# Performance work log

Measured on AMD Instinct MI355X. Metric: run time of the kernel, lower is better.

## Reference

```python
import jax, jax.numpy as jnp
import numpy as np

M = 8192          # flattened tokens (batch*seq)
IN_FEATURES = 4096
OUT_FEATURES = 4096


def setup_inputs() -> dict:
    key = jax.random.key(0)
    k1, k2, k3 = jax.random.split(key, 3)
    # int8-valued activations and weights, stored as int32 (values in [-128, 127])
    x = jax.random.randint(k1, (M, IN_FEATURES), -128, 128, dtype=jnp.int32)
    int_weight = jax.random.randint(k2, (OUT_FEATURES, IN_FEATURES), -128, 127, dtype=jnp.int32)
    bias = (jax.random.normal(k3, (OUT_FEATURES,), dtype=jnp.float32) * 0.02).astype(jnp.float16)
    return {"x": x, "int_weight": int_weight, "bias": bias}


def reference(x, int_weight, bias):
    # x.to(torch.int8); quik int8Matmul: int8 GEMM with int32 accumulation, out = x @ W^T
    x_i8 = x.astype(jnp.int8)
    w_i8 = int_weight.astype(jnp.int8)
    acc = jax.lax.dot_general(
        x_i8, w_i8,
        dimension_numbers=(((1,), (1,)), ((), ())),  # [M, K] x [N, K] -> [M, N]
        preferred_element_type=jnp.int32,
    )
    # .to(torch.float16) then bias add (fused epilogue target)
    return acc.astype(jnp.float16) + bias
```

## Files before the change

kernel.cpp:

```cpp
#include <hip/hip_runtime.h>

#define MDIM 8192
#define NDIM 4096
#define KDIM 4096
#define BM 256
#define BN 128
#define BK 128

typedef int v4i __attribute__((ext_vector_type(4)));
typedef int v16i __attribute__((ext_vector_type(16)));

__device__ __forceinline__ unsigned pack4(int x, int y, int z, int w) {
    return (unsigned)(x & 0xff) | ((unsigned)(y & 0xff) << 8) |
           ((unsigned)(z & 0xff) << 16) | ((unsigned)w << 24);
}

__global__ __launch_bounds__(256) void pack_tiled(const int* __restrict__ x,
                                                  const int* __restrict__ w,
                                                  uint4* __restrict__ xp,
                                                  uint4* __restrict__ wp) {
    __shared__ unsigned lds32[256 * 33];
    const int wg  = blockIdx.x;
    const int tid = threadIdx.x;
    const int kq   = tid & 31;
    const int rsub = tid >> 5;

    if (wg < 1024) {
        const int mtile = wg >> 5, kiter = wg & 31;
        const int* base = x + (size_t)(mtile * 256) * KDIM + kiter * 128;
#pragma unroll
        for (int it = 0; it < 32; ++it) {
            const int row = it * 8 + rsub;
            int4 v = *(const int4*)(base + (size_t)row * KDIM + kq * 4);
            lds32[row * 33 + kq] = pack4(v.x, v.y, v.z, v.w);
        }
        __syncthreads();
        uint4* dst = xp + (size_t)(mtile * 32 + kiter) * 2048;
#pragma unroll
        for (int it = 0; it < 8; ++it) {
            const int g = it * 256 + tid;
            const int kb = g >> 8, row = g & 255;
            const unsigned* p = &lds32[row * 33 + kb * 4];
            uint4 o;
            o.x = p[0]; o.y = p[1]; o.z = p[2]; o.w = p[3];
            dst[g] = o;
        }
    } else {
        const int ntile = (wg - 1024) >> 5, kiter = wg & 31;
        const int* base = w + (size_t)(ntile * 128) * KDIM + kiter * 128;
#pragma unroll
        for (int it = 0; it < 16; ++it) {
            const int row = it * 8 + rsub;
            int4 v = *(const int4*)(base + (size_t)row * KDIM + kq * 4);
            lds32[row * 33 + kq] = pack4(v.x, v.y, v.z, v.w);
        }
        __syncthreads();
        uint4* dst = wp + (size_t)(ntile * 32 + kiter) * 1024;
#pragma unroll
        for (int it = 0; it < 4; ++it) {
            const int g  = it * 256 + tid;
            const int ln = g & 63, h = g >> 6;
            const int wc2 = h >> 3, nt = (h >> 2) & 1, ks = h & 3;
            const int row = wc2 * 64 + nt * 32 + (ln & 31);
            const int kb  = 2 * ks + (ln >> 5);
            const unsigned* p = &lds32[row * 33 + kb * 4];
            uint4 o;
            o.x = p[0]; o.y = p[1]; o.z = p[2]; o.w = p[3];
            dst[g] = o;
        }
    }
}

template <bool PACKED>
__global__ __launch_bounds__(256, 2) void gemm_i8(const char* __restrict__ Ap,
                                                  const char* __restrict__ Bp,
                                                  const int* __restrict__ A32,
                                                  const int* __restrict__ B32,
                                                  const _Float16* __restrict__ bias,
                                                  _Float16* __restrict__ out) {
    __shared__ char lds[32768];

    const int tid  = threadIdx.x;
    const int lane = tid & 63;
    const int wave = tid >> 6;
    const int bm0 = blockIdx.y * BM;
    const int bn0 = blockIdx.x * BN;
    const int wr  = wave >> 1;
    const int wc  = wave & 1;
    const int l31 = lane & 31;
    const int kg  = lane >> 5;

    const char* apan = Ap + (size_t)blockIdx.y * (BM * KDIM) + lane * 16;
    const char* bpan = Bp + (size_t)blockIdx.x * (BN * KDIM) + wc * 8192 + lane * 16;

    int aoffs[8];
    if constexpr (!PACKED) {
#pragma unroll
        for (int r = 0; r < 8; ++r) {
            const int c = r * 4 + wave;
            aoffs[r] = (bm0 + (c & 3) * 64 + lane) * KDIM + (c >> 2) * 16;
        }
    }

    int abase[4];
#pragma unroll
    for (int mt = 0; mt < 4; ++mt)
        abase[mt] = kg * 4096 + (wr * 128 + mt * 32 + l31) * 16;

    v16i acc[4][2];
#pragma unroll
    for (int mt = 0; mt < 4; ++mt)
#pragma unroll
        for (int nt = 0; nt < 2; ++nt)
#pragma unroll
            for (int i = 0; i < 16; ++i) acc[mt][nt][i] = 0;

    for (int k0 = 0; k0 < KDIM; k0 += BK) {
        v4i bf[2][4];
        if constexpr (PACKED) {
#pragma unroll
            for (int r = 0; r < 8; ++r) {
                const int c = r * 4 + wave;
                __builtin_amdgcn_global_load_lds(
                    (__attribute__((address_space(1))) void*)(apan + c * 1024),
                    (__attribute__((address_space(3))) void*)(lds + c * 1024), 16, 0, 0);
            }
#pragma unroll
            for (int nt = 0; nt < 2; ++nt)
#pragma unroll
                for (int ks = 0; ks < 4; ++ks)
                    bf[nt][ks] = *(const v4i*)(bpan + (nt * 4 + ks) * 1024);
            apan += BM * BK;
            bpan += BN * BK;
        } else {
#pragma unroll
            for (int r = 0; r < 8; ++r) {
                const int c = r * 4 + wave;
                const int4* s = (const int4*)(A32 + (size_t)aoffs[r]);
                int4 v0 = s[0], v1 = s[1], v2 = s[2], v3 = s[3];
                uint4 pk;
                pk.x = pack4(v0.x, v0.y, v0.z, v0.w);
                pk.y = pack4(v1.x, v1.y, v1.z, v1.w);
                pk.z = pack4(v2.x, v2.y, v2.z, v2.w);
                pk.w = pack4(v3.x, v3.y, v3.z, v3.w);
                *(uint4*)(lds + c * 1024 + lane * 16) = pk;
                aoffs[r] += BK;
            }
#pragma unroll
            for (int nt = 0; nt < 2; ++nt)
#pragma unroll
                for (int ks = 0; ks < 4; ++ks) {
                    const int* s = B32 + (size_t)(bn0 + wc * 64 + nt * 32 + l31) * KDIM
                                   + k0 + (2 * ks + kg) * 16;
                    int4 v0 = ((const int4*)s)[0], v1 = ((const int4*)s)[1];
                    int4 v2 = ((const int4*)s)[2], v3 = ((const int4*)s)[3];
                    bf[nt][ks][0] = (int)pack4(v0.x, v0.y, v0.z, v0.w);
                    bf[nt][ks][1] = (int)pack4(v1.x, v1.y, v1.z, v1.w);
                    bf[nt][ks][2] = (int)pack4(v2.x, v2.y, v2.z, v2.w);
                    bf[nt][ks][3] = (int)pack4(v3.x, v3.y, v3.z, v3.w);
                }
        }
        __syncthreads();

#pragma unroll
        for (int ks = 0; ks < 4; ++ks) {
            v4i af[4];
#pragma unroll
            for (int mt = 0; mt < 4; ++mt)
                af[mt] = *(const v4i*)(lds + abase[mt] + ks * 8192);
#pragma unroll
            for (int mt = 0; mt < 4; ++mt)
#pragma unroll
                for (int nt = 0; nt < 2; ++nt)
                    acc[mt][nt] = __builtin_amdgcn_mfma_i32_32x32x32_i8(
                        af[mt], bf[nt][ks], acc[mt][nt], 0, 0, 0);
        }

        __syncthreads();
    }

    const _Float16 bv0 = bias[bn0 + wc * 64 + l31];
    const _Float16 bv1 = bias[bn0 + wc * 64 + 32 + l31];
#pragma unroll
    for (int mt = 0; mt < 4; ++mt) {
#pragma unroll
        for (int nt = 0; nt < 2; ++nt) {
            const int gcol = bn0 + wc * 64 + nt * 32 + l31;
            const _Float16 bb = nt ? bv1 : bv0;
#pragma unroll
            for (int r = 0; r < 16; ++r) {
                const int rit  = (r & 3) + 8 * (r >> 2) + 4 * kg;
                const int grow = bm0 + wr * 128 + mt * 32 + rit;
                _Float16 h = (_Float16)(float)acc[mt][nt][r] + bb;
                out[(size_t)grow * NDIM + gcol] = h;
            }
        }
    }
}

extern "C" void kernel_launch(void* const* d_in, const int* in_sizes, int n_in,
                              void* d_out, int out_size, void* d_ws, size_t ws_size,
                              hipStream_t stream) {
    const int* x = (const int*)d_in[0];
    const int* w = (const int*)d_in[1];
    const _Float16* bias = (const _Float16*)d_in[2];
    _Float16* out = (_Float16*)d_out;

    const size_t xbytes = (size_t)MDIM * KDIM;
    const size_t wbytes = (size_t)NDIM * KDIM;

    if (ws_size >= xbytes + wbytes) {
        char* xp = (char*)d_ws;
        char* wp = xp + xbytes;
        pack_tiled<<<2048, 256, 0, stream>>>(x, w, (uint4*)xp, (uint4*)wp);
        gemm_i8<true><<<dim3(NDIM / BN, MDIM / BM), 256, 0, stream>>>(
            xp, wp, nullptr, nullptr, bias, out);
    } else {
        gemm_i8<false><<<dim3(NDIM / BN, MDIM / BM), 256, 0, stream>>>(
            nullptr, nullptr, x, w, bias, out);
    }
}
```

Measured before the change: 396.8 us.

## Double-buffer A tile in LDS and prefetch B registers across K iterations

Makes the packed GEMM main loop double-buffered. The A tile goes into two 32KB LDS halves through async global_load_lds, and the B fragments are prefetched into a second register set while the current tile is computed. The aim is to hide global memory latency behind the MFMA work and to drop one barrier per iteration. In exchange, LDS per block doubles to 64KB and register pressure rises, which may limit the 2-blocks-per-CU occupancy target. There is also a possible race, since compute does not wait on vmcnt for the async LDS loads other than through the barrier.

```diff
diff --git a/kernel.cpp b/kernel.cpp
--- a/kernel.cpp
+++ b/kernel.cpp
@@ -78,7 +78,7 @@
                                                   const int* __restrict__ B32,
                                                   const _Float16* __restrict__ bias,
                                                   _Float16* __restrict__ out) {
-    __shared__ char lds[32768];
+    __shared__ char lds[65536];
 
     const int tid  = threadIdx.x;
     const int lane = tid & 63;
@@ -93,46 +93,87 @@
     const char* apan = Ap + (size_t)blockIdx.y * (BM * KDIM) + lane * 16;
     const char* bpan = Bp + (size_t)blockIdx.x * (BN * KDIM) + wc * 8192 + lane * 16;
 
-    int aoffs[8];
-    if constexpr (!PACKED) {
+    int abase[4];
+#pragma unroll
+    for (int mt = 0; mt < 4; ++mt)
+        abase[mt] = kg * 4096 + (wr * 128 + mt * 32 + l31) * 16;
+
+    v16i acc[4][2];
+#pragma unroll
+    for (int mt = 0; mt < 4; ++mt)
+#pragma unroll
+        for (int nt = 0; nt < 2; ++nt)
+#pragma unroll
+            for (int i = 0; i < 16; ++i) acc[mt][nt][i] = 0;
+
+    auto issueA = [&](char* buf, const char* pan) {
+#pragma unroll
+        for (int r = 0; r < 8; ++r) {
+            const int c = r * 4 + wave;
+            __builtin_amdgcn_global_load_lds(
+                (__attribute__((address_space(1))) void*)(pan + c * 1024),
+                (__attribute__((address_space(3))) void*)(buf + c * 1024), 16, 0, 0);
+        }
+    };
+    auto loadB = [&](v4i (&bf)[2][4], const char* pan) {
+#pragma unroll
+        for (int nt = 0; nt < 2; ++nt)
+#pragma unroll
+            for (int ks = 0; ks < 4; ++ks)
+                bf[nt][ks] = *(const v4i*)(pan + (nt * 4 + ks) * 1024);
+    };
+    auto compute = [&](const char* buf, const v4i (&bf)[2][4]) {
+#pragma unroll
+        for (int ks = 0; ks < 4; ++ks) {
+            v4i af[4];
+#pragma unroll
+            for (int mt = 0; mt < 4; ++mt)
+                af[mt] = *(const v4i*)(buf + abase[mt] + ks * 8192);
+#pragma unroll
+            for (int mt = 0; mt < 4; ++mt)
+#pragma unroll
+                for (int nt = 0; nt < 2; ++nt)
+                    acc[mt][nt] = __builtin_amdgcn_mfma_i32_32x32x32_i8(
+                        af[mt], bf[nt][ks], acc[mt][nt], 0, 0, 0);
+        }
+    };
+
+    if constexpr (PACKED) {
+        v4i bf0[2][4], bf1[2][4];
+        issueA(lds, apan);
+        apan += BM * BK;
+        loadB(bf0, bpan);
+        bpan += BN * BK;
+#pragma unroll 1
+        for (int p = 0; p < 15; ++p) {
+            __syncthreads();
+            issueA(lds + 32768, apan);
+            apan += BM * BK;
+            loadB(bf1, bpan);
+            bpan += BN * BK;
+            compute(lds, bf0);
+            __syncthreads();
+            issueA(lds, apan);
+            apan += BM * BK;
+            loadB(bf0, bpan);
+            bpan += BN * BK;
+            compute(lds + 32768, bf1);
+        }
+        __syncthreads();
+        issueA(lds + 32768, apan);
+        loadB(bf1, bpan);
+        compute(lds, bf0);
+        __syncthreads();
+        compute(lds + 32768, bf1);
+    } else {
+        int aoffs[8];
 #pragma unroll
         for (int r = 0; r < 8; ++r) {
             const int c = r * 4 + wave;
             aoffs[r] = (bm0 + (c & 3) * 64 + lane) * KDIM + (c >> 2) * 16;
         }
-    }
-
-    int abase[4];
-#pragma unroll
-    for (int mt = 0; mt < 4; ++mt)
-        abase[mt] = kg * 4096 + (wr * 128 + mt * 32 + l31) * 16;
-
-    v16i acc[4][2];
-#pragma unroll
-    for (int mt = 0; mt < 4; ++mt)
-#pragma unroll
-        for (int nt = 0; nt < 2; ++nt)
-#pragma unroll
-            for (int i = 0; i < 16; ++i) acc[mt][nt][i] = 0;
-
-    for (int k0 = 0; k0 < KDIM; k0 += BK) {
-        v4i bf[2][4];
-        if constexpr (PACKED) {
-#pragma unroll
-            for (int r = 0; r < 8; ++r) {
-                const int c = r * 4 + wave;
-                __builtin_amdgcn_global_load_lds(
-                    (__attribute__((address_space(1))) void*)(apan + c * 1024),
-                    (__attribute__((address_space(3))) void*)(lds + c * 1024), 16, 0, 0);
-            }
-#pragma unroll
-            for (int nt = 0; nt < 2; ++nt)
-#pragma unroll
-                for (int ks = 0; ks < 4; ++ks)
-                    bf[nt][ks] = *(const v4i*)(bpan + (nt * 4 + ks) * 1024);
-            apan += BM * BK;
-            bpan += BN * BK;
-        } else {
+        for (int k0 = 0; k0 < KDIM; k0 += BK) {
+            v4i bfx[2][4];
 #pragma unroll
             for (int r = 0; r < 8; ++r) {
                 const int c = r * 4 + wave;
@@ -154,29 +195,15 @@
                                    + k0 + (2 * ks + kg) * 16;
                     int4 v0 = ((const int4*)s)[0], v1 = ((const int4*)s)[1];
                     int4 v2 = ((const int4*)s)[2], v3 = ((const int4*)s)[3];
-                    bf[nt][ks][0] = (int)pack4(v0.x, v0.y, v0.z, v0.w);
-                    bf[nt][ks][1] = (int)pack4(v1.x, v1.y, v1.z, v1.w);
-                    bf[nt][ks][2] = (int)pack4(v2.x, v2.y, v2.z, v2.w);
-                    bf[nt][ks][3] = (int)pack4(v3.x, v3.y, v3.z, v3.w);
+                    bfx[nt][ks][0] = (int)pack4(v0.x, v0.y, v0.z, v0.w);
+                    bfx[nt][ks][1] = (int)pack4(v1.x, v1.y, v1.z, v1.w);
+                    bfx[nt][ks][2] = (int)pack4(v2.x, v2.y, v2.z, v2.w);
+                    bfx[nt][ks][3] = (int)pack4(v3.x, v3.y, v3.z, v3.w);
                 }
-        }
-        __syncthreads();
-
-#pragma unroll
-        for (int ks = 0; ks < 4; ++ks) {
-            v4i af[4];
-#pragma unroll
-            for (int mt = 0; mt < 4; ++mt)
-                af[mt] = *(const v4i*)(lds + abase[mt] + ks * 8192);
-#pragma unroll
-            for (int mt = 0; mt < 4; ++mt)
-#pragma unroll
-                for (int nt = 0; nt < 2; ++nt)
-                    acc[mt][nt] = __builtin_amdgcn_mfma_i32_32x32x32_i8(
-                        af[mt], bf[nt][ks], acc[mt][nt], 0, 0, 0);
-        }
-
-        __syncthreads();
+            __syncthreads();
+            compute(lds, bfx);
+            __syncthreads();
+        }
     }
 
     const _Float16 bv0 = bias[bn0 + wc * 64 + l31];
```

Result: faster. 386.8 us (-2.5%).
